# Kernel tuning notes

Hardware: AMD Instinct MI355X
Metric: run time of the kernel (lower is better)

The kernel has to match this reference:

```python
import jax, jax.numpy as jnp
import numpy as np

TEMP = 0.5
EPS = 1e-8  # matches torch F.cosine_similarity eps clamp


def setup_inputs() -> dict:
    key = jax.random.key(0)
    k1, k2 = jax.random.split(key)
    B, D = 8192, 512
    v = jax.random.normal(k1, (B, D), dtype=jnp.float32)
    u = jax.random.normal(k2, (B, D), dtype=jnp.float32)
    return {"v": v, "u": u}


def _normalize(x):
    n = jnp.sqrt(jnp.sum(x * x, axis=-1, keepdims=True))
    return x / jnp.maximum(n, EPS)


def reference(v, u):
    # Fused form of the original nested-loop NT-Xent-style loss.
    vn = _normalize(v)                      # [B, D]
    un = _normalize(u)                      # [B, D]
    sim = jnp.einsum('bd,cd->bc', vn, un)   # [B, B] pairwise cosine similarity
    diag = jnp.einsum('bd,bd->b', vn, un)   # cos(v_i, u_i)
    numerator = jnp.exp(diag / TEMP)        # [B]
    # original: denominator = numerator.detach().clone(); then += sum_j exp(sim[i,j]/T)
    denominator = jax.lax.stop_gradient(numerator) + jnp.sum(jnp.exp(sim / TEMP), axis=1)
    loss = -jnp.log(numerator / denominator)
    return loss
```

## Files before the change

### kernel.cpp

```cpp
#include <hip/hip_runtime.h>

typedef int   int4v  __attribute__((ext_vector_type(4)));
typedef char  char8v __attribute__((ext_vector_type(8)));

#define NROWS 8192
#define DIM 512
#define ROWB 512
#define NT 4
#define SWEEP 4

#define AS1(p) ((const __attribute__((address_space(1))) void*)(p))
#define AS3(p) ((__attribute__((address_space(3))) void*)(p))

#if __has_builtin(__builtin_amdgcn_exp2f)
#define EXP2(x) __builtin_amdgcn_exp2f(x)
#else
#define EXP2(x) exp2f(x)
#endif

__global__ __launch_bounds__(256) void prep_kernel(
    const float* __restrict__ v, const float* __restrict__ u,
    char* __restrict__ vq, char* __restrict__ uq,
    float* __restrict__ sa, float* __restrict__ sb,
    float* __restrict__ diag, float* __restrict__ rowsum)
{
    const int row  = blockIdx.x * 4 + (threadIdx.x >> 6);
    const int lane = threadIdx.x & 63;
    const float4* vr = reinterpret_cast<const float4*>(v + (size_t)row * DIM);
    const float4* ur = reinterpret_cast<const float4*>(u + (size_t)row * DIM);
    const float4 a0 = vr[lane * 2], a1 = vr[lane * 2 + 1];
    const float4 b0 = ur[lane * 2], b1 = ur[lane * 2 + 1];
    float av[8] = {a0.x, a0.y, a0.z, a0.w, a1.x, a1.y, a1.z, a1.w};
    float bv[8] = {b0.x, b0.y, b0.z, b0.w, b1.x, b1.y, b1.z, b1.w};
    float sv = 0.f, su = 0.f, sd = 0.f, mv = 0.f, mu = 0.f;
#pragma unroll
    for (int i = 0; i < 8; ++i) {
        sv += av[i] * av[i];
        su += bv[i] * bv[i];
        sd += av[i] * bv[i];
        mv = fmaxf(mv, fabsf(av[i]));
        mu = fmaxf(mu, fabsf(bv[i]));
    }
#pragma unroll
    for (int m = 32; m; m >>= 1) {
        sv += __shfl_xor(sv, m);
        su += __shfl_xor(su, m);
        sd += __shfl_xor(sd, m);
        mv = fmaxf(mv, __shfl_xor(mv, m));
        mu = fmaxf(mu, __shfl_xor(mu, m));
    }
    const float rv = 1.0f / fmaxf(sqrtf(sv), 1e-8f);
    const float ru = 1.0f / fmaxf(sqrtf(su), 1e-8f);
    const float qv = 127.0f / fmaxf(mv, 1e-20f);
    const float qu = 127.0f / fmaxf(mu, 1e-20f);
    char8v cv, cu;
#pragma unroll
    for (int i = 0; i < 8; ++i) {
        cv[i] = (char)__float2int_rn(av[i] * qv);
        cu[i] = (char)__float2int_rn(bv[i] * qu);
    }
    reinterpret_cast<char8v*>(vq + (size_t)row * DIM)[lane] = cv;
    reinterpret_cast<char8v*>(uq + (size_t)row * DIM)[lane] = cu;
    if (lane == 0) {
        sa[row] = mv * rv / 127.0f;
        sb[row] = mu * ru / 127.0f;
        diag[row] = sd * rv * ru;
        rowsum[row] = 0.0f;
    }
}

__global__ __launch_bounds__(256, 2) void simsum_kernel(
    const char* __restrict__ A, const char* __restrict__ Bm,
    const float* __restrict__ sa, const float* __restrict__ sb,
    float* __restrict__ rowsum)
{
    __shared__ __align__(16) char ldsB[2][16384];
    const int tid  = threadIdx.x;
    const int wave = tid >> 6;
    const int lane = tid & 63;
    const int ln15 = lane & 15;
    const int lhi  = lane >> 4;
    const int swz  = (ln15 & 7) << 4;

    const int brow = blockIdx.x;
    const int bgrp = blockIdx.y;
    const int growA = brow * 128 + wave * 32;
    const int gcol0 = bgrp * (SWEEP * 128);

    const char* gA = A;
    const char* gB = Bm;

    int4v Areg[NT][2][2];
#pragma unroll
    for (int t = 0; t < NT; ++t)
#pragma unroll
        for (int kk = 0; kk < 2; ++kk)
#pragma unroll
            for (int m = 0; m < 2; ++m) {
                const int r = growA + m * 16 + ln15;
                Areg[t][kk][m] = *reinterpret_cast<const int4v*>(
                    gA + (size_t)r * ROWB + t * 128 + kk * 64 + lhi * 16);
            }

    const float C2 = 2.885390081777927f;
    float ga[2][4];
#pragma unroll
    for (int m = 0; m < 2; ++m)
#pragma unroll
        for (int rr = 0; rr < 4; ++rr)
            ga[m][rr] = sa[growA + m * 16 + lhi * 4 + rr] * C2;

    float rs[2][4];
#pragma unroll
    for (int m = 0; m < 2; ++m)
#pragma unroll
        for (int rr = 0; rr < 4; ++rr)
            rs[m][rr] = 0.f;

    const int r0   = tid >> 3;
    const int sl16 = (((tid & 7) ^ ((tid >> 3) & 7)) << 4);

    auto stageB = [&](int buf, int s, int t) {
#pragma unroll
        for (int g = 0; g < 4; ++g) {
            const int r = g * 32 + r0;
            __builtin_amdgcn_global_load_lds(
                AS1(gB + (size_t)(gcol0 + s * 128 + r) * ROWB + t * 128 + sl16),
                AS3(&ldsB[buf][g * 4096 + tid * 16]), 16, 0, 0);
        }
    };

    stageB(0, 0, 0);
    __syncthreads();

    int buf = 0;
    for (int s = 0; s < SWEEP; ++s) {
        int4v acc[2][8];
#pragma unroll
        for (int m = 0; m < 2; ++m)
#pragma unroll
            for (int n = 0; n < 8; ++n)
                acc[m][n] = (int4v){0, 0, 0, 0};

#pragma unroll
        for (int t = 0; t < NT; ++t) {
            const int nx = s * 4 + t + 1;
            if (nx < SWEEP * 4) stageB(buf ^ 1, nx >> 2, nx & 3);
#pragma unroll
            for (int kk = 0; kk < 2; ++kk) {
                int4v Bf[8];
#pragma unroll
                for (int n = 0; n < 8; ++n) {
                    const int r = n * 16 + ln15;
                    Bf[n] = *reinterpret_cast<const int4v*>(
                        &ldsB[buf][r * 128 + ((kk * 64 + lhi * 16) ^ swz)]);
                }
#pragma unroll
                for (int m = 0; m < 2; ++m)
#pragma unroll
                    for (int n = 0; n < 8; ++n)
                        acc[m][n] = __builtin_amdgcn_mfma_i32_16x16x64_i8(
                            Areg[t][kk][m], Bf[n], acc[m][n], 0, 0, 0);
            }
            __syncthreads();
            buf ^= 1;
        }

        float sbv[8];
#pragma unroll
        for (int n = 0; n < 8; ++n)
            sbv[n] = sb[gcol0 + s * 128 + n * 16 + ln15];
#pragma unroll
        for (int m = 0; m < 2; ++m)
#pragma unroll
            for (int rr = 0; rr < 4; ++rr) {
                const float g = ga[m][rr];
#pragma unroll
                for (int n = 0; n < 8; ++n)
                    rs[m][rr] += EXP2((float)acc[m][n][rr] * g * sbv[n]);
            }
    }

#pragma unroll
    for (int m = 0; m < 2; ++m)
#pragma unroll
        for (int rr = 0; rr < 4; ++rr) {
            float s = rs[m][rr];
            s += __shfl_xor(s, 1);
            s += __shfl_xor(s, 2);
            s += __shfl_xor(s, 4);
            s += __shfl_xor(s, 8);
            if (ln15 == 0)
                atomicAdd(&rowsum[growA + m * 16 + lhi * 4 + rr], s);
        }
}

__global__ __launch_bounds__(256) void loss_kernel(
    const float* __restrict__ diag, const float* __restrict__ rowsum,
    float* __restrict__ out)
{
    const int i = blockIdx.x * 256 + threadIdx.x;
    const float d2 = diag[i] * 2.0f;
    out[i] = logf(expf(d2) + rowsum[i]) - d2;
}

extern "C" void kernel_launch(void* const* d_in, const int* in_sizes, int n_in,
                              void* d_out, int out_size, void* d_ws, size_t ws_size,
                              hipStream_t stream) {
    const float* v = (const float*)d_in[0];
    const float* u = (const float*)d_in[1];
    float* out = (float*)d_out;
    char* ws = (char*)d_ws;
    char*  vq     = ws;
    char*  uq     = ws + (size_t)4194304;
    float* sa     = (float*)(ws + (size_t)8388608);
    float* sb     = (float*)(ws + (size_t)8388608 + 32768);
    float* diag   = (float*)(ws + (size_t)8388608 + 65536);
    float* rowsum = (float*)(ws + (size_t)8388608 + 98304);

    prep_kernel<<<NROWS / 4, 256, 0, stream>>>(v, u, vq, uq, sa, sb, diag, rowsum);
    dim3 grid(64, 16);
    simsum_kernel<<<grid, 256, 0, stream>>>(vq, uq, sa, sb, rowsum);
    loss_kernel<<<NROWS / 256, 256, 0, stream>>>(diag, rowsum, out);
}
```

Before: 55.64 us.

## Pack A into MFMA fragment layout and stream it from global per step

The prep kernel now writes the quantized v matrix in a pre-swizzled layout so that each lane's MFMA A-fragment is one contiguous 16-byte load. The sim kernel no longer keeps all of A in registers. It streams the A fragments from global (cache) for each k-step and reshapes the wave tile from 32x128 to 64x64, using a smaller B LDS tile and a 32x32 grid. The aim is to cut register pressure and the amount of B staged through LDS. The cost is repeated global/L2 loads of A inside the inner loop.

```diff
diff --git a/kernel.cpp b/kernel.cpp
--- a/kernel.cpp
+++ b/kernel.cpp
@@ -20,7 +20,7 @@
 
 __global__ __launch_bounds__(256) void prep_kernel(
     const float* __restrict__ v, const float* __restrict__ u,
-    char* __restrict__ vq, char* __restrict__ uq,
+    char* __restrict__ apack, char* __restrict__ uq,
     float* __restrict__ sa, float* __restrict__ sb,
     float* __restrict__ diag, float* __restrict__ rowsum)
 {
@@ -59,7 +59,11 @@
         cv[i] = (char)__float2int_rn(av[i] * qv);
         cu[i] = (char)__float2int_rn(bv[i] * qu);
     }
-    reinterpret_cast<char8v*>(vq + (size_t)row * DIM)[lane] = cv;
+    const size_t dst = (size_t)(row >> 4) * 8192 + (lane >> 4) * 2048 +
+                       ((lane >> 3) & 1) * 1024 +
+                       ((((lane >> 1) & 3) * 16 + (row & 15)) * 16) +
+                       (lane & 1) * 8;
+    *reinterpret_cast<char8v*>(apack + dst) = cv;
     reinterpret_cast<char8v*>(uq + (size_t)row * DIM)[lane] = cu;
     if (lane == 0) {
         sa[row] = mv * rv / 127.0f;
@@ -70,11 +74,11 @@
 }
 
 __global__ __launch_bounds__(256, 2) void simsum_kernel(
-    const char* __restrict__ A, const char* __restrict__ Bm,
+    const char* __restrict__ Apack, const char* __restrict__ Bq,
     const float* __restrict__ sa, const float* __restrict__ sb,
     float* __restrict__ rowsum)
 {
-    __shared__ __align__(16) char ldsB[2][16384];
+    __shared__ __align__(16) char ldsB[2][8192];
     const int tid  = threadIdx.x;
     const int wave = tid >> 6;
     const int lane = tid & 63;
@@ -84,35 +88,21 @@
 
     const int brow = blockIdx.x;
     const int bgrp = blockIdx.y;
-    const int growA = brow * 128 + wave * 32;
-    const int gcol0 = bgrp * (SWEEP * 128);
-
-    const char* gA = A;
-    const char* gB = Bm;
-
-    int4v Areg[NT][2][2];
-#pragma unroll
-    for (int t = 0; t < NT; ++t)
-#pragma unroll
-        for (int kk = 0; kk < 2; ++kk)
-#pragma unroll
-            for (int m = 0; m < 2; ++m) {
-                const int r = growA + m * 16 + ln15;
-                Areg[t][kk][m] = *reinterpret_cast<const int4v*>(
-                    gA + (size_t)r * ROWB + t * 128 + kk * 64 + lhi * 16);
-            }
+    const int growA = brow * 256 + wave * 64;
+    const int gcol0 = bgrp * (SWEEP * 64);
+    const char* abase = Apack + (size_t)(growA >> 4) * 8192;
 
     const float C2 = 2.885390081777927f;
-    float ga[2][4];
-#pragma unroll
-    for (int m = 0; m < 2; ++m)
+    float ga[4][4];
+#pragma unroll
+    for (int m = 0; m < 4; ++m)
 #pragma unroll
         for (int rr = 0; rr < 4; ++rr)
             ga[m][rr] = sa[growA + m * 16 + lhi * 4 + rr] * C2;
 
-    float rs[2][4];
-#pragma unroll
-    for (int m = 0; m < 2; ++m)
+    float rs[4][4];
+#pragma unroll
+    for (int m = 0; m < 4; ++m)
 #pragma unroll
         for (int rr = 0; rr < 4; ++rr)
             rs[m][rr] = 0.f;
@@ -120,69 +110,74 @@
     const int r0   = tid >> 3;
     const int sl16 = (((tid & 7) ^ ((tid >> 3) & 7)) << 4);
 
-    auto stageB = [&](int buf, int s, int t) {
-#pragma unroll
-        for (int g = 0; g < 4; ++g) {
-            const int r = g * 32 + r0;
+    auto stageB = [&](int buf, int ct, int t) {
+#pragma unroll
+        for (int g = 0; g < 2; ++g) {
+            const int col = ct * 64 + g * 32 + r0;
             __builtin_amdgcn_global_load_lds(
-                AS1(gB + (size_t)(gcol0 + s * 128 + r) * ROWB + t * 128 + sl16),
+                AS1(Bq + (size_t)col * ROWB + t * 128 + sl16),
                 AS3(&ldsB[buf][g * 4096 + tid * 16]), 16, 0, 0);
         }
     };
 
-    stageB(0, 0, 0);
+    stageB(0, bgrp * SWEEP, 0);
     __syncthreads();
 
     int buf = 0;
     for (int s = 0; s < SWEEP; ++s) {
-        int4v acc[2][8];
-#pragma unroll
-        for (int m = 0; m < 2; ++m)
-#pragma unroll
-            for (int n = 0; n < 8; ++n)
+        int4v acc[4][4];
+#pragma unroll
+        for (int m = 0; m < 4; ++m)
+#pragma unroll
+            for (int n = 0; n < 4; ++n)
                 acc[m][n] = (int4v){0, 0, 0, 0};
 
 #pragma unroll
         for (int t = 0; t < NT; ++t) {
-            const int nx = s * 4 + t + 1;
-            if (nx < SWEEP * 4) stageB(buf ^ 1, nx >> 2, nx & 3);
+            const int nx = s * NT + t + 1;
+            if (nx < SWEEP * NT) stageB(buf ^ 1, bgrp * SWEEP + (nx >> 2), nx & 3);
 #pragma unroll
             for (int kk = 0; kk < 2; ++kk) {
-                int4v Bf[8];
-#pragma unroll
-                for (int n = 0; n < 8; ++n) {
-                    const int r = n * 16 + ln15;
+                int4v Af[4], Bf[4];
+#pragma unroll
+                for (int m = 0; m < 4; ++m)
+                    Af[m] = *reinterpret_cast<const int4v*>(
+                        abase + (size_t)m * 8192 + t * 2048 + kk * 1024 +
+                        lane * 16);
+#pragma unroll
+                for (int n = 0; n < 4; ++n) {
+                    const int c = n * 16 + ln15;
                     Bf[n] = *reinterpret_cast<const int4v*>(
-                        &ldsB[buf][r * 128 + ((kk * 64 + lhi * 16) ^ swz)]);
+                        &ldsB[buf][c * 128 + ((kk * 64 + lhi * 16) ^ swz)]);
                 }
 #pragma unroll
-                for (int m = 0; m < 2; ++m)
-#pragma unroll
-                    for (int n = 0; n < 8; ++n)
+                for (int m = 0; m < 4; ++m)
+#pragma unroll
+                    for (int n = 0; n < 4; ++n)
                         acc[m][n] = __builtin_amdgcn_mfma_i32_16x16x64_i8(
-                            Areg[t][kk][m], Bf[n], acc[m][n], 0, 0, 0);
+                            Af[m], Bf[n], acc[m][n], 0, 0, 0);
             }
             __syncthreads();
             buf ^= 1;
         }
 
-        float sbv[8];
-#pragma unroll
-        for (int n = 0; n < 8; ++n)
-            sbv[n] = sb[gcol0 + s * 128 + n * 16 + ln15];
-#pragma unroll
-        for (int m = 0; m < 2; ++m)
+        float sbv[4];
+#pragma unroll
+        for (int n = 0; n < 4; ++n)
+            sbv[n] = sb[gcol0 + s * 64 + n * 16 + ln15];
+#pragma unroll
+        for (int m = 0; m < 4; ++m)
 #pragma unroll
             for (int rr = 0; rr < 4; ++rr) {
                 const float g = ga[m][rr];
 #pragma unroll
-                for (int n = 0; n < 8; ++n)
+                for (int n = 0; n < 4; ++n)
                     rs[m][rr] += EXP2((float)acc[m][n][rr] * g * sbv[n]);
             }
     }
 
 #pragma unroll
-    for (int m = 0; m < 2; ++m)
+    for (int m = 0; m < 4; ++m)
 #pragma unroll
         for (int rr = 0; rr < 4; ++rr) {
             float s = rs[m][rr];
@@ -211,15 +206,15 @@
     const float* u = (const float*)d_in[1];
     float* out = (float*)d_out;
     char* ws = (char*)d_ws;
-    char*  vq     = ws;
+    char*  apack  = ws;
     char*  uq     = ws + (size_t)4194304;
     float* sa     = (float*)(ws + (size_t)8388608);
     float* sb     = (float*)(ws + (size_t)8388608 + 32768);
     float* diag   = (float*)(ws + (size_t)8388608 + 65536);
     float* rowsum = (float*)(ws + (size_t)8388608 + 98304);
 
-    prep_kernel<<<NROWS / 4, 256, 0, stream>>>(v, u, vq, uq, sa, sb, diag, rowsum);
-    dim3 grid(64, 16);
-    simsum_kernel<<<grid, 256, 0, stream>>>(vq, uq, sa, sb, rowsum);
+    prep_kernel<<<NROWS / 4, 256, 0, stream>>>(v, u, apack, uq, sa, sb, diag, rowsum);
+    dim3 grid(32, 32);
+    simsum_kernel<<<grid, 256, 0, stream>>>(apack, uq, sa, sb, rowsum);
     loss_kernel<<<NROWS / 256, 256, 0, stream>>>(diag, rowsum, out);
 }
```

After: 85.24 us. +53.2%, slower.

## Deepen B-tile LDS pipeline to four buffers and double sweep per block

Applied to the files above, without the earlier changes.

Raises the number of B column tiles each block sweeps from four to eight and halves the grid, so the register-resident A fragments are reused over more columns and fewer atomics are issued. Replaces the double-buffered LDS staging with a four-slot ring that prefetches two tiles ahead. __syncthreads is replaced with explicit s_waitcnt vmcnt plus s_barrier, so compute can overlap outstanding global-to-LDS loads. In exchange LDS use doubles to 64KB per block, which may limit blocks per CU, and the grid shrinks to 512 blocks. The hand-placed waitcnt/barrier ordering must be exactly right for correctness.

```diff
diff --git a/kernel.cpp b/kernel.cpp
--- a/kernel.cpp
+++ b/kernel.cpp
@@ -7,7 +7,7 @@
 #define DIM 512
 #define ROWB 512
 #define NT 4
-#define SWEEP 4
+#define SWEEP 8
 
 #define AS1(p) ((const __attribute__((address_space(1))) void*)(p))
 #define AS3(p) ((__attribute__((address_space(3))) void*)(p))
@@ -70,11 +70,11 @@
 }
 
 __global__ __launch_bounds__(256, 2) void simsum_kernel(
-    const char* __restrict__ A, const char* __restrict__ Bm,
+    const char* __restrict__ A, const char* __restrict__ Bq,
     const float* __restrict__ sa, const float* __restrict__ sb,
     float* __restrict__ rowsum)
 {
-    __shared__ __align__(16) char ldsB[2][16384];
+    __shared__ __align__(16) char ldsB[4][16384];
     const int tid  = threadIdx.x;
     const int wave = tid >> 6;
     const int lane = tid & 63;
@@ -88,7 +88,7 @@
     const int gcol0 = bgrp * (SWEEP * 128);
 
     const char* gA = A;
-    const char* gB = Bm;
+    const char* gB = Bq;
 
     int4v Areg[NT][2][2];
 #pragma unroll
@@ -120,20 +120,23 @@
     const int r0   = tid >> 3;
     const int sl16 = (((tid & 7) ^ ((tid >> 3) & 7)) << 4);
 
-    auto stageB = [&](int buf, int s, int t) {
-#pragma unroll
-        for (int g = 0; g < 4; ++g) {
-            const int r = g * 32 + r0;
+    auto stageB = [&](int bi, int gs) {
+        const int ct = gs >> 2;
+        const int kt = gs & 3;
+#pragma unroll
+        for (int q = 0; q < 4; ++q) {
+            const int col = gcol0 + ct * 128 + q * 32 + r0;
             __builtin_amdgcn_global_load_lds(
-                AS1(gB + (size_t)(gcol0 + s * 128 + r) * ROWB + t * 128 + sl16),
-                AS3(&ldsB[buf][g * 4096 + tid * 16]), 16, 0, 0);
+                AS1(gB + (size_t)col * ROWB + kt * 128 + sl16),
+                AS3(&ldsB[bi][q * 4096 + tid * 16]), 16, 0, 0);
         }
     };
 
-    stageB(0, 0, 0);
-    __syncthreads();
-
-    int buf = 0;
+    stageB(0, 0);
+    stageB(1, 1);
+    asm volatile("s_waitcnt vmcnt(4)" ::: "memory");
+    asm volatile("s_barrier" ::: "memory");
+
     for (int s = 0; s < SWEEP; ++s) {
         int4v acc[2][8];
 #pragma unroll
@@ -143,27 +146,28 @@
                 acc[m][n] = (int4v){0, 0, 0, 0};
 
 #pragma unroll
-        for (int t = 0; t < NT; ++t) {
-            const int nx = s * 4 + t + 1;
-            if (nx < SWEEP * 4) stageB(buf ^ 1, nx >> 2, nx & 3);
+        for (int tt = 0; tt < NT; ++tt) {
+            const int g = s * 4 + tt;
+            if (g + 2 < 32) stageB((tt + 2) & 3, g + 2);
 #pragma unroll
             for (int kk = 0; kk < 2; ++kk) {
                 int4v Bf[8];
 #pragma unroll
                 for (int n = 0; n < 8; ++n) {
-                    const int r = n * 16 + ln15;
+                    const int c = n * 16 + ln15;
                     Bf[n] = *reinterpret_cast<const int4v*>(
-                        &ldsB[buf][r * 128 + ((kk * 64 + lhi * 16) ^ swz)]);
+                        &ldsB[tt & 3][c * 128 + ((kk * 64 + lhi * 16) ^ swz)]);
                 }
 #pragma unroll
                 for (int m = 0; m < 2; ++m)
 #pragma unroll
                     for (int n = 0; n < 8; ++n)
                         acc[m][n] = __builtin_amdgcn_mfma_i32_16x16x64_i8(
-                            Areg[t][kk][m], Bf[n], acc[m][n], 0, 0, 0);
+                            Areg[tt][kk][m], Bf[n], acc[m][n], 0, 0, 0);
             }
-            __syncthreads();
-            buf ^= 1;
+            if (g < 30)       asm volatile("s_waitcnt vmcnt(4)" ::: "memory");
+            else if (g == 30) asm volatile("s_waitcnt vmcnt(0)" ::: "memory");
+            if (g < 31)       asm volatile("s_barrier" ::: "memory");
         }
 
         float sbv[8];
@@ -174,10 +178,10 @@
         for (int m = 0; m < 2; ++m)
 #pragma unroll
             for (int rr = 0; rr < 4; ++rr) {
-                const float g = ga[m][rr];
+                const float g2 = ga[m][rr];
 #pragma unroll
                 for (int n = 0; n < 8; ++n)
-                    rs[m][rr] += EXP2((float)acc[m][n][rr] * g * sbv[n]);
+                    rs[m][rr] += EXP2((float)acc[m][n][rr] * g2 * sbv[n]);
             }
     }
 
@@ -219,7 +223,7 @@
     float* rowsum = (float*)(ws + (size_t)8388608 + 98304);
 
     prep_kernel<<<NROWS / 4, 256, 0, stream>>>(v, u, vq, uq, sa, sb, diag, rowsum);
-    dim3 grid(64, 16);
+    dim3 grid(64, 8);
     simsum_kernel<<<grid, 256, 0, stream>>>(vq, uq, sa, sb, rowsum);
     loss_kernel<<<NROWS / 256, 256, 0, stream>>>(diag, rowsum, out);
 }
```

Result: faster. 52.21 us, median of 3 (-6.2%).
